# Performance work log

Hardware: AMD Instinct MI355X
Metric: run time of the kernel (lower is better)

The kernel has to match this reference:

```python
import jax, jax.numpy as jnp
import numpy as np
from jax import lax

B, H, W, Q, C = 2, 96, 96, 30000, 64
DIMS = [C * 9 + 4, 256, 256, 256, 256, 3]  # imnet MLP


def setup_inputs() -> dict:
    key = jax.random.key(0)
    ks = jax.random.split(key, 20)
    d = {}
    d["inp"] = jax.random.normal(ks[0], (B, 3, H, W), jnp.float32)
    d["coord"] = jax.random.uniform(ks[1], (B, Q, 2), jnp.float32) * 2.0 - 1.0
    d["cell"] = jax.random.uniform(ks[2], (B, Q, 2), jnp.float32) * (2.0 / 256.0)
    d["conv_w"] = jax.random.normal(ks[3], (C, 3, 3, 3), jnp.float32) * 0.1
    d["conv_b"] = jnp.zeros((C,), jnp.float32)
    for i in range(5):
        fan_in = DIMS[i]
        d[f"w{i}"] = jax.random.normal(ks[4 + i], (DIMS[i], DIMS[i + 1]), jnp.float32) / np.sqrt(fan_in)
        d[f"b{i}"] = jnp.zeros((DIMS[i + 1],), jnp.float32)
    return d


def _liif_forward(inp, coord, cell, conv_w, conv_b, ws, bs):
    # encoder: 3x3 conv + tanh (gen_feat)
    feat = lax.conv_general_dilated(inp, conv_w, (1, 1), "SAME",
                                    dimension_numbers=("NCHW", "OIHW", "NCHW"))
    feat = jnp.tanh(feat + conv_b[None, :, None, None])  # [B,C,H,W]
    b, c, h, w = feat.shape

    # feat_unfold: F.unfold(feat, 3, padding=1) -> [B, C*9, H, W]
    pad = jnp.pad(feat, ((0, 0), (0, 0), (1, 1), (1, 1)))
    patches = jnp.stack([pad[:, :, i:i + h, j:j + w] for i in range(3) for j in range(3)], axis=2)
    fu = patches.reshape(b, c * 9, h, w).transpose(0, 2, 3, 1)  # [B,H,W,9C]

    # local ensemble offsets
    offsets = jnp.array([[-1., -1.], [-1., 1.], [1., -1.], [1., 1.]], jnp.float32)
    rad = jnp.array([1.0 / h, 1.0 / w], jnp.float32)  # 2/r/2
    eps = 1e-6
    ec = coord[None] + (offsets * rad)[:, None, None, :] + eps  # [4,B,Q,2]
    ec = jnp.clip(ec, -1 + 1e-10, 1 - 1e-10)

    # grid_sample nearest, align_corners=False: ix = ((x+1)*size - 1)/2, round
    iy = jnp.clip(jnp.round((ec[..., 0] + 1) * h / 2 - 0.5).astype(jnp.int32), 0, h - 1)
    ix = jnp.clip(jnp.round((ec[..., 1] + 1) * w / 2 - 0.5).astype(jnp.int32), 0, w - 1)
    b_idx = jnp.arange(b)[None, :, None]  # [1,B,1]
    q_feat = fu[b_idx, iy, ix]  # [4,B,Q,9C]

    # feat_coord (make_coord): pixel-center coords in [-1,1]
    yc = (-1.0 + (2.0 * jnp.arange(h, dtype=jnp.float32) + 1.0) / h)
    xc = (-1.0 + (2.0 * jnp.arange(w, dtype=jnp.float32) + 1.0) / w)
    fc = jnp.stack(jnp.meshgrid(yc, xc, indexing="ij"), axis=-1)  # [H,W,2]
    q_coord = fc[iy, ix]  # [4,B,Q,2]

    scale = jnp.array([h, w], jnp.float32)
    rel_coord = (coord[None] - q_coord) * scale  # [4,B,Q,2]
    rel_cell = cell * scale  # [B,Q,2]

    x = jnp.concatenate(
        [q_feat, rel_coord, jnp.broadcast_to(rel_cell[None], rel_coord.shape)], axis=-1)  # [4,B,Q,580]

    # imnet MLP
    for wi, bi in zip(ws[:-1], bs[:-1]):
        x = jax.nn.relu(x @ wi + bi)
    x = x @ ws[-1] + bs[-1]  # [4,B,Q,3]

    areas = jnp.abs(jnp.prod(rel_coord, axis=-1, keepdims=True)) + 1e-9
    areas = areas / jnp.sum(areas, axis=0, keepdims=True)
    areas = areas[::-1]  # swap diagonal ensemble weights

    out = jnp.sum(x * areas, axis=0)  # [B,Q,3]
    return jnp.tanh(out) * 1.01  # fat_tanh(eps=0.01)


def reference(inp, coord, cell, conv_w, conv_b, w0, b0, w1, b1, w2, b2, w3, b3, w4, b4):
    return _liif_forward(inp, coord, cell, conv_w, conv_b,
                         [w0, w1, w2, w3, w4], [b0, b1, b2, b3, b4])
```

## Files before the change

kernel.cpp:

```cpp
#include <hip/hip_runtime.h>


typedef _Float16 half8   __attribute__((ext_vector_type(8)));
typedef _Float16 half4v  __attribute__((ext_vector_type(4)));
typedef _Float16 half2v  __attribute__((ext_vector_type(2)));
typedef float    float4v __attribute__((ext_vector_type(4)));
typedef float    floatx16 __attribute__((ext_vector_type(16)));

__device__ __forceinline__ _Float16 to_h(float v) {
  return (_Float16)fminf(fmaxf(v, -60000.0f), 60000.0f);
}

#define NQ 30000
#define QT 469
#define QTP 472

__global__ void prep_kernel(const float* __restrict__ w0,
                            const float* __restrict__ w1,
                            const float* __restrict__ w2,
                            const float* __restrict__ w3,
                            const float* __restrict__ w4,
                            _Float16* __restrict__ p0, _Float16* __restrict__ p1,
                            _Float16* __restrict__ p2, _Float16* __restrict__ p3,
                            _Float16* __restrict__ p4) {
  int idx = blockIdx.x * 256 + threadIdx.x;
  if (idx < 18944) {
    int kb = idx >> 8, n = idx & 255;
    half8 hv;
#pragma unroll
    for (int i = 0; i < 8; ++i) {
      int f = kb * 8 + i;
      float v = 0.0f;
      if (f < 576)      v = w0[((f & 63) * 9 + (f >> 6)) * 256 + n];
      else if (f < 580) v = w0[f * 256 + n];
      hv[i] = (_Float16)v;
    }
    *(half8*)(p0 + idx * 8) = hv;
  } else if (idx < 43520) {
    int j = idx - 18944;
    int l = j >> 13;
    int j2 = j & 8191;
    int kb = j2 >> 8, n = j2 & 255;
    const float* w = (l == 0) ? w1 : (l == 1) ? w2 : w3;
    _Float16* p = (l == 0) ? p1 : (l == 1) ? p2 : p3;
    half8 hv;
#pragma unroll
    for (int i = 0; i < 8; ++i)
      hv[i] = (_Float16)w[(kb * 8 + i) * 256 + n];
    *(half8*)(p + j2 * 8) = hv;
  } else if (idx < 44032) {
    int j = idx - 43520;
    int kb = j >> 4, n = j & 15;
    half8 hv;
#pragma unroll
    for (int i = 0; i < 8; ++i) {
      float v = (n < 3) ? w4[(kb * 8 + i) * 3 + n] : 0.0f;
      hv[i] = (_Float16)v;
    }
    *(half8*)(p4 + j * 8) = hv;
  }
}

__global__ void conv_kernel(const float* __restrict__ inp,
                            const float* __restrict__ cw,
                            const float* __restrict__ cb,
                            _Float16* __restrict__ P) {
  __shared__ __align__(16) float s_w[1728];
  __shared__ __align__(16) float s_b[64];
  for (int i = threadIdx.x; i < 1728; i += 256) s_w[i] = cw[i];
  if (threadIdx.x < 64) s_b[threadIdx.x] = cb[threadIdx.x];
  __syncthreads();
  int tid = blockIdx.x * 256 + threadIdx.x;
  if (tid >= 2 * 98 * 98) return;
  int b = tid / 9604;
  int rem = tid % 9604;
  int yy = rem / 98, xx = rem % 98;
  alignas(16) _Float16 outv[64];
  if (yy == 0 || yy == 97 || xx == 0 || xx == 97) {
#pragma unroll
    for (int c = 0; c < 64; ++c) outv[c] = (_Float16)0.0f;
  } else {
    int y = yy - 1, x = xx - 1;
    float win[27];
#pragma unroll
    for (int ci = 0; ci < 3; ++ci)
#pragma unroll
      for (int ky = 0; ky < 3; ++ky)
#pragma unroll
        for (int kx = 0; kx < 3; ++kx) {
          int yi = y + ky - 1, xi = x + kx - 1;
          float v = 0.0f;
          if (yi >= 0 && yi < 96 && xi >= 0 && xi < 96)
            v = inp[((b * 3 + ci) * 96 + yi) * 96 + xi];
          win[ci * 9 + ky * 3 + kx] = v;
        }
    for (int co = 0; co < 64; ++co) {
      float acc = s_b[co];
#pragma unroll
      for (int k = 0; k < 27; ++k) acc = fmaf(win[k], s_w[co * 27 + k], acc);
      outv[co] = (_Float16)tanhf(acc);
    }
  }
  _Float16* dst = P + tid * 64;
#pragma unroll
  for (int j = 0; j < 8; ++j) ((half8*)dst)[j] = ((const half8*)outv)[j];
}

__global__ __launch_bounds__(256, 1) void gmat_kernel(
    const _Float16* __restrict__ P,
    const _Float16* __restrict__ wp0,
    _Float16* __restrict__ G) {
  __shared__ __align__(16) _Float16 s_p[3][98][68];

  const int t    = threadIdx.x;
  const int lane = t & 63;
  const int wv   = t >> 6;
  const int ln32 = lane & 31;
  const int hi   = lane >> 5;
  const int blk  = blockIdx.x;
  const int bb   = (blk & 4) >> 2;
  const int y    = (blk >> 3) * 4 + (blk & 3);

  const int rowbase = (bb * 98 + y) * 98 * 64;
  for (int j = t; j < 2352; j += 256) {
    int row = j / 784;
    int jr  = j - row * 784;
    int px  = jr >> 3;
    int ci  = jr & 7;
    half8 v = *(const half8*)(P + rowbase + row * 6272 + jr * 8);
    *(half8*)(&s_p[row][px][ci * 8]) = v;
  }
  __syncthreads();

  const _Float16* wb0 = wp0 + (hi * 256 + wv * 64 + ln32) * 8;

  floatx16 acc[2][3];
#pragma unroll
  for (int mt2 = 0; mt2 < 2; ++mt2)
#pragma unroll
    for (int nt = 0; nt < 3; ++nt) acc[mt2][nt] = (floatx16)(0.0f);

  half8 afA[2], afB[2];
  afA[0] = *(const half8*)(wb0);          afA[1] = *(const half8*)(wb0 + 256);
  afB[0] = *(const half8*)(wb0 + 4096);   afB[1] = *(const half8*)(wb0 + 4096 + 256);

#pragma unroll 1
  for (int s = 0; s < 36; s += 2) {
    {
      const int patch = s >> 2;
      const int py = patch / 3, px = patch % 3;
      const int cb = ((s & 3) << 4) + hi * 8;
      half8 bf[3];
#pragma unroll
      for (int nt = 0; nt < 3; ++nt)
        bf[nt] = *(const half8*)(&s_p[py][nt * 32 + ln32 + px][cb]);
#pragma unroll
      for (int mt2 = 0; mt2 < 2; ++mt2)
#pragma unroll
        for (int nt = 0; nt < 3; ++nt)
          acc[mt2][nt] = __builtin_amdgcn_mfma_f32_32x32x16_f16(
              afA[mt2], bf[nt], acc[mt2][nt], 0, 0, 0);
      const int sp = (s + 2 <= 35) ? (s + 2) : 35;
      afA[0] = *(const half8*)(wb0 + sp * 4096);
      afA[1] = *(const half8*)(wb0 + sp * 4096 + 256);
    }
    {
      const int s1 = s + 1;
      const int patch = s1 >> 2;
      const int py = patch / 3, px = patch % 3;
      const int cb = ((s1 & 3) << 4) + hi * 8;
      half8 bf[3];
#pragma unroll
      for (int nt = 0; nt < 3; ++nt)
        bf[nt] = *(const half8*)(&s_p[py][nt * 32 + ln32 + px][cb]);
#pragma unroll
      for (int mt2 = 0; mt2 < 2; ++mt2)
#pragma unroll
        for (int nt = 0; nt < 3; ++nt)
          acc[mt2][nt] = __builtin_amdgcn_mfma_f32_32x32x16_f16(
              afB[mt2], bf[nt], acc[mt2][nt], 0, 0, 0);
      const int sp = (s + 3 <= 35) ? (s + 3) : 35;
      afB[0] = *(const half8*)(wb0 + sp * 4096);
      afB[1] = *(const half8*)(wb0 + sp * 4096 + 256);
    }
  }
  const int gybase = ((bb * 98 + y) * 98) * 256;
#pragma unroll
  for (int mt2 = 0; mt2 < 2; ++mt2)
#pragma unroll
    for (int nt = 0; nt < 3; ++nt) {
      half8 c0, c1;
#pragma unroll
      for (int j = 0; j < 8; ++j) {
        c0[j] = (_Float16)acc[mt2][nt][j];
        c1[j] = (_Float16)acc[mt2][nt][8 + j];
      }
      _Float16* ga = G + gybase + (nt * 32 + ln32) * 256 + (wv * 2 + mt2) * 32 + hi * 16;
      *(half8*)(ga)     = c0;
      *(half8*)(ga + 8) = c1;
    }
}

__device__ __forceinline__ void writeback32(floatx16 (&acc)[2][4],
                                            const float* __restrict__ sb,
                                            _Float16 (*s_h)[264],
                                            int wv, int ln32, int hi) {
#pragma unroll
  for (int mt2 = 0; mt2 < 2; ++mt2) {
    const int mb = wv * 64 + mt2 * 32 + 4 * hi;
#pragma unroll
    for (int g = 0; g < 4; ++g) {
      const int m0 = mb + 8 * g;
      float b0 = sb[m0], b1 = sb[m0 + 1], b2 = sb[m0 + 2], b3 = sb[m0 + 3];
#pragma unroll
      for (int nt2 = 0; nt2 < 4; ++nt2) {
        const int n = nt2 * 32 + ln32;
        float v0 = fmaxf(acc[mt2][nt2][4 * g + 0] + b0, 0.0f);
        float v1 = fmaxf(acc[mt2][nt2][4 * g + 1] + b1, 0.0f);
        float v2 = fmaxf(acc[mt2][nt2][4 * g + 2] + b2, 0.0f);
        float v3 = fmaxf(acc[mt2][nt2][4 * g + 3] + b3, 0.0f);
        half2v lo  = __builtin_bit_cast(half2v, __builtin_amdgcn_cvt_pkrtz(v0, v1));
        half2v hi2 = __builtin_bit_cast(half2v, __builtin_amdgcn_cvt_pkrtz(v2, v3));
        half4v hv;
        hv[0] = lo[0]; hv[1] = lo[1]; hv[2] = hi2[0]; hv[3] = hi2[1];
        *(half4v*)(&s_h[n][m0]) = hv;
      }
    }
  }
}

__device__ __forceinline__ void layer256(const _Float16* __restrict__ wbl,
                                         _Float16 (*s_h)[264],
                                         int ln32, int hi,
                                         floatx16 (&acc)[2][4]) {
#pragma unroll
  for (int mt2 = 0; mt2 < 2; ++mt2)
#pragma unroll
    for (int nt2 = 0; nt2 < 4; ++nt2) acc[mt2][nt2] = (floatx16)(0.0f);
  half8 afA[2], afB[2], bfA[4], bfB[4];
  afA[0] = *(const half8*)(wbl);
  afA[1] = *(const half8*)(wbl + 256);
  afB[0] = *(const half8*)(wbl + 4096);
  afB[1] = *(const half8*)(wbl + 4096 + 256);
#pragma unroll
  for (int nt2 = 0; nt2 < 4; ++nt2) {
    bfA[nt2] = *(const half8*)(&s_h[nt2 * 32 + ln32][hi * 8]);
    bfB[nt2] = *(const half8*)(&s_h[nt2 * 32 + ln32][16 + hi * 8]);
  }
#pragma unroll 1
  for (int s = 0; s < 16; s += 2) {
#pragma unroll
    for (int mt2 = 0; mt2 < 2; ++mt2)
#pragma unroll
      for (int nt2 = 0; nt2 < 4; ++nt2)
        acc[mt2][nt2] = __builtin_amdgcn_mfma_f32_32x32x16_f16(
            afA[mt2], bfA[nt2], acc[mt2][nt2], 0, 0, 0);
    {
      const int sc = (s + 2 < 16) ? (s + 2) : 0;
      const int sw = (s + 2 < 16) ? (s + 2) : 15;
      afA[0] = *(const half8*)(wbl + sw * 4096);
      afA[1] = *(const half8*)(wbl + sw * 4096 + 256);
#pragma unroll
      for (int nt2 = 0; nt2 < 4; ++nt2)
        bfA[nt2] = *(const half8*)(&s_h[nt2 * 32 + ln32][sc * 16 + hi * 8]);
    }
#pragma unroll
    for (int mt2 = 0; mt2 < 2; ++mt2)
#pragma unroll
      for (int nt2 = 0; nt2 < 4; ++nt2)
        acc[mt2][nt2] = __builtin_amdgcn_mfma_f32_32x32x16_f16(
            afB[mt2], bfB[nt2], acc[mt2][nt2], 0, 0, 0);
    {
      const int sc = (s + 3 < 16) ? (s + 3) : 0;
      const int sw = (s + 3 < 16) ? (s + 3) : 15;
      afB[0] = *(const half8*)(wbl + sw * 4096);
      afB[1] = *(const half8*)(wbl + sw * 4096 + 256);
#pragma unroll
      for (int nt2 = 0; nt2 < 4; ++nt2)
        bfB[nt2] = *(const half8*)(&s_h[nt2 * 32 + ln32][sc * 16 + hi * 8]);
    }
  }
}

__global__ __launch_bounds__(256, 2) void liif_main(
    const float* __restrict__ coord, const float* __restrict__ cell,
    const float* __restrict__ bias0, const float* __restrict__ bias1,
    const float* __restrict__ bias2, const float* __restrict__ bias3,
    const float* __restrict__ bias4,
    const _Float16* __restrict__ G,
    const _Float16* __restrict__ wp0, const _Float16* __restrict__ wp1,
    const _Float16* __restrict__ wp2, const _Float16* __restrict__ wp3,
    const _Float16* __restrict__ wp4,
    float* __restrict__ out) {
  __shared__ __align__(16) int      s_pix[4][64];
  __shared__ __align__(16) float    s_area[4][64];
  __shared__ __align__(16) _Float16 s_ext[4][64][8];
  __shared__ __align__(16) float    s_bias[1028];
  __shared__ __align__(16) float    s_out[128][4];
  __shared__ __align__(16) float    s_num[64][4];
  __shared__ __align__(16) _Float16 s_h[128][264];

  const int t   = threadIdx.x;
  const int blk = blockIdx.x;
  const int bb  = (blk & 4) >> 2;
  const int tile = (blk >> 3) * 4 + (blk & 3);
  const int q0  = tile * 64;

  for (int i = t; i < 1027; i += 256) {
    float v;
    if (i < 256)       v = bias0[i];
    else if (i < 512)  v = bias1[i - 256];
    else if (i < 768)  v = bias2[i - 512];
    else if (i < 1024) v = bias3[i - 768];
    else               v = bias4[i - 1024];
    s_bias[i] = v;
  }

  if (t < 64) {
    int q = q0 + t;
    bool valid = q < NQ;
    float c0 = 0.f, c1 = 0.f, e0 = 0.f, e1 = 0.f;
    if (valid) {
      int base = (bb * NQ + q) * 2;
      c0 = coord[base]; c1 = coord[base + 1];
      e0 = cell[base];  e1 = cell[base + 1];
    }
    float rc0 = e0 * 96.0f, rc1 = e1 * 96.0f;
#pragma unroll
    for (int o = 0; o < 4; ++o) {
      float oy = (o < 2) ? -1.0f : 1.0f;
      float ox = (o & 1) ? 1.0f : -1.0f;
      float ec0 = (c0 + oy * (1.0f / 96.0f)) + 1e-6f;
      float ec1 = (c1 + ox * (1.0f / 96.0f)) + 1e-6f;
      ec0 = fminf(fmaxf(ec0, -1.0f), 1.0f);
      ec1 = fminf(fmaxf(ec1, -1.0f), 1.0f);
      int iy = (int)rintf(((ec0 + 1.0f) * 96.0f) * 0.5f - 0.5f);
      int ix = (int)rintf(((ec1 + 1.0f) * 96.0f) * 0.5f - 0.5f);
      iy = min(max(iy, 0), 95); ix = min(max(ix, 0), 95);
      float qc0 = -1.0f + (2.0f * (float)iy + 1.0f) / 96.0f;
      float qc1 = -1.0f + (2.0f * (float)ix + 1.0f) / 96.0f;
      float r0 = (c0 - qc0) * 96.0f;
      float r1 = (c1 - qc1) * 96.0f;
      s_pix[o][t]  = (bb * 98 + iy) * 98 + ix;
      s_area[o][t] = fabsf(r0 * r1) + 1e-9f;
      s_ext[o][t][0] = to_h(r0);  s_ext[o][t][1] = to_h(r1);
      s_ext[o][t][2] = to_h(rc0); s_ext[o][t][3] = to_h(rc1);
      s_ext[o][t][4] = (_Float16)0.0f; s_ext[o][t][5] = (_Float16)0.0f;
      s_ext[o][t][6] = (_Float16)0.0f; s_ext[o][t][7] = (_Float16)0.0f;
    }
    s_num[t][0] = 0.f; s_num[t][1] = 0.f; s_num[t][2] = 0.f; s_num[t][3] = 0.f;
  }
  __syncthreads();

  const int lane = t & 63;
  const int wv   = t >> 6;
  const int ln32 = lane & 31;
  const int hi   = lane >> 5;
  const int ln16 = lane & 15;
  const int lg   = lane >> 4;

  const _Float16* wb0 = wp0 + (hi * 256 + wv * 64 + ln32) * 8;
  const _Float16* wb1 = wp1 + (hi * 256 + wv * 64 + ln32) * 8;
  const _Float16* wb2 = wp2 + (hi * 256 + wv * 64 + ln32) * 8;
  const _Float16* wb3 = wp3 + (hi * 256 + wv * 64 + ln32) * 8;

#pragma unroll 1
  for (int p = 0; p < 2; ++p) {
    int pixr[4]; int eidx[4];
#pragma unroll
    for (int nt2 = 0; nt2 < 4; ++nt2) {
      int r = nt2 * 32 + ln32;
      int o = p * 2 + (r >> 6);
      int q = r & 63;
      pixr[nt2] = s_pix[o][q];
      eidx[nt2] = (o * 64 + q) * 8;
    }

    floatx16 acc[2][4];
#pragma unroll
    for (int mt2 = 0; mt2 < 2; ++mt2)
#pragma unroll
      for (int nt2 = 0; nt2 < 4; ++nt2) {
        const _Float16* ga = G + pixr[nt2] * 256 + (wv * 2 + mt2) * 32 + hi * 16;
        half8 g0 = *(const half8*)(ga);
        half8 g1 = *(const half8*)(ga + 8);
        floatx16 a;
#pragma unroll
        for (int j = 0; j < 8; ++j) {
          a[j]     = (float)g0[j];
          a[8 + j] = (float)g1[j];
        }
        acc[mt2][nt2] = a;
      }
    {
      half8 ae[2];
      ae[0] = *(const half8*)(wb0 + 36 * 4096);
      ae[1] = *(const half8*)(wb0 + 36 * 4096 + 256);
      half8 z = {(_Float16)0, (_Float16)0, (_Float16)0, (_Float16)0,
                 (_Float16)0, (_Float16)0, (_Float16)0, (_Float16)0};
      half8 bfe[4];
#pragma unroll
      for (int nt2 = 0; nt2 < 4; ++nt2)
        bfe[nt2] = (hi == 0) ? *(const half8*)(&s_ext[0][0][0] + eidx[nt2]) : z;
#pragma unroll
      for (int mt2 = 0; mt2 < 2; ++mt2)
#pragma unroll
        for (int nt2 = 0; nt2 < 4; ++nt2)
          acc[mt2][nt2] = __builtin_amdgcn_mfma_f32_32x32x16_f16(
              ae[mt2], bfe[nt2], acc[mt2][nt2], 0, 0, 0);
    }
    writeback32(acc, s_bias, s_h, wv, ln32, hi);
    __syncthreads();

    layer256(wb1, s_h, ln32, hi, acc);
    __syncthreads();
    writeback32(acc, s_bias + 256, s_h, wv, ln32, hi);
    __syncthreads();

    layer256(wb2, s_h, ln32, hi, acc);
    __syncthreads();
    writeback32(acc, s_bias + 512, s_h, wv, ln32, hi);
    __syncthreads();

    layer256(wb3, s_h, ln32, hi, acc);
    __syncthreads();
    writeback32(acc, s_bias + 768, s_h, wv, ln32, hi);
    __syncthreads();

    half8 af4 = *(const half8*)(wp4 + (lg * 16 + ln16) * 8);
    float4v a4[2];
    a4[0] = (float4v){0.f, 0.f, 0.f, 0.f};
    a4[1] = (float4v){0.f, 0.f, 0.f, 0.f};
#pragma unroll 1
    for (int s = 0; s < 8; ++s) {
      half8 afc = af4;
      if (s < 7)
        af4 = *(const half8*)(wp4 + (((s + 1) * 4 + lg) * 16 + ln16) * 8);
#pragma unroll
      for (int u = 0; u < 2; ++u) {
        int row = (2 * wv + u) * 16 + ln16;
        half8 bf = *(const half8*)(&s_h[row][s * 32 + lg * 8]);
        a4[u] = __builtin_amdgcn_mfma_f32_16x16x32_f16(afc, bf, a4[u], 0, 0, 0);
      }
    }
    if (lg == 0) {
#pragma unroll
      for (int u = 0; u < 2; ++u) {
        int row = (2 * wv + u) * 16 + ln16;
        *(float4v*)(&s_out[row][0]) = a4[u];
      }
    }
    __syncthreads();

    if (t < 64) {
      float a_lo = s_area[3 - 2 * p][t];
      float a_hi = s_area[2 - 2 * p][t];
#pragma unroll
      for (int j = 0; j < 3; ++j)
        s_num[t][j] += s_out[t][j] * a_lo + s_out[64 + t][j] * a_hi;
    }
  }

  if (t < 64) {
    int q = q0 + t;
    if (q < NQ) {
      float den = s_area[0][t] + s_area[1][t] + s_area[2][t] + s_area[3][t];
      int ob = (bb * NQ + q) * 3;
#pragma unroll
      for (int j = 0; j < 3; ++j) {
        float v = s_num[t][j] / den + s_bias[1024 + j];
        out[ob + j] = tanhf(v) * 1.01f;
      }
    }
  }
}

extern "C" void kernel_launch(void* const* d_in, const int* in_sizes, int n_in,
                              void* d_out, int out_size, void* d_ws, size_t ws_size,
                              hipStream_t stream) {
  const float* inp   = (const float*)d_in[0];
  const float* coord = (const float*)d_in[1];
  const float* cell  = (const float*)d_in[2];
  const float* cw    = (const float*)d_in[3];
  const float* cb    = (const float*)d_in[4];
  const float* w0    = (const float*)d_in[5];
  const float* b0    = (const float*)d_in[6];
  const float* w1    = (const float*)d_in[7];
  const float* b1    = (const float*)d_in[8];
  const float* w2    = (const float*)d_in[9];
  const float* b2    = (const float*)d_in[10];
  const float* w3    = (const float*)d_in[11];
  const float* b3    = (const float*)d_in[12];
  const float* w4    = (const float*)d_in[13];
  const float* b4    = (const float*)d_in[14];

  char* ws = (char*)d_ws;
  _Float16* P   = (_Float16*)(ws);
  _Float16* wp0 = (_Float16*)(ws + 2458624);
  _Float16* wp1 = (_Float16*)(ws + 2761728);
  _Float16* wp2 = (_Float16*)(ws + 2892800);
  _Float16* wp3 = (_Float16*)(ws + 3023872);
  _Float16* wp4 = (_Float16*)(ws + 3154944);
  _Float16* G   = (_Float16*)(ws + 3163136);
  float* outp = (float*)d_out;

  hipLaunchKernelGGL(prep_kernel, dim3(172), dim3(256), 0, stream,
                     w0, w1, w2, w3, w4, wp0, wp1, wp2, wp3, wp4);
  hipLaunchKernelGGL(conv_kernel, dim3(76), dim3(256), 0, stream, inp, cw, cb, P);
  hipLaunchKernelGGL(gmat_kernel, dim3(192), dim3(256), 0, stream, P, wp0, G);
  hipLaunchKernelGGL(liif_main, dim3(8 * (QTP / 4)), dim3(256), 0, stream,
                     coord, cell, b0, b1, b2, b3, b4,
                     G, wp0, wp1, wp2, wp3, wp4, outp);
}
```

Before: 268.4 us.

## Process one ensemble offset per pass to halve tile and raise occupancy

Each MLP pass now covers 64 query rows (one ensemble offset) instead of 128 (two offsets), and the loop runs four times instead of two. Accumulator registers and the s_h/s_out shared buffers are halved, and launch bounds go from 2 to 3 blocks per SM. The aim is more resident waves to hide latency. The cost is double the barriers and loop iterations, and each weight fragment loaded is reused across fewer MFMAs.

```diff
diff --git a/kernel.cpp b/kernel.cpp
--- a/kernel.cpp
+++ b/kernel.cpp
@@ -201,7 +201,7 @@
     }
 }
 
-__device__ __forceinline__ void writeback32(floatx16 (&acc)[2][4],
+__device__ __forceinline__ void writeback32(floatx16 (&acc)[2][2],
                                             const float* __restrict__ sb,
                                             _Float16 (*s_h)[264],
                                             int wv, int ln32, int hi) {
@@ -213,7 +213,7 @@
       const int m0 = mb + 8 * g;
       float b0 = sb[m0], b1 = sb[m0 + 1], b2 = sb[m0 + 2], b3 = sb[m0 + 3];
 #pragma unroll
-      for (int nt2 = 0; nt2 < 4; ++nt2) {
+      for (int nt2 = 0; nt2 < 2; ++nt2) {
         const int n = nt2 * 32 + ln32;
         float v0 = fmaxf(acc[mt2][nt2][4 * g + 0] + b0, 0.0f);
         float v1 = fmaxf(acc[mt2][nt2][4 * g + 1] + b1, 0.0f);
@@ -232,18 +232,18 @@
 __device__ __forceinline__ void layer256(const _Float16* __restrict__ wbl,
                                          _Float16 (*s_h)[264],
                                          int ln32, int hi,
-                                         floatx16 (&acc)[2][4]) {
+                                         floatx16 (&acc)[2][2]) {
 #pragma unroll
   for (int mt2 = 0; mt2 < 2; ++mt2)
 #pragma unroll
-    for (int nt2 = 0; nt2 < 4; ++nt2) acc[mt2][nt2] = (floatx16)(0.0f);
-  half8 afA[2], afB[2], bfA[4], bfB[4];
+    for (int nt2 = 0; nt2 < 2; ++nt2) acc[mt2][nt2] = (floatx16)(0.0f);
+  half8 afA[2], afB[2], bfA[2], bfB[2];
   afA[0] = *(const half8*)(wbl);
   afA[1] = *(const half8*)(wbl + 256);
   afB[0] = *(const half8*)(wbl + 4096);
   afB[1] = *(const half8*)(wbl + 4096 + 256);
 #pragma unroll
-  for (int nt2 = 0; nt2 < 4; ++nt2) {
+  for (int nt2 = 0; nt2 < 2; ++nt2) {
     bfA[nt2] = *(const half8*)(&s_h[nt2 * 32 + ln32][hi * 8]);
     bfB[nt2] = *(const half8*)(&s_h[nt2 * 32 + ln32][16 + hi * 8]);
   }
@@ -252,7 +252,7 @@
 #pragma unroll
     for (int mt2 = 0; mt2 < 2; ++mt2)
 #pragma unroll
-      for (int nt2 = 0; nt2 < 4; ++nt2)
+      for (int nt2 = 0; nt2 < 2; ++nt2)
         acc[mt2][nt2] = __builtin_amdgcn_mfma_f32_32x32x16_f16(
             afA[mt2], bfA[nt2], acc[mt2][nt2], 0, 0, 0);
     {
@@ -261,13 +261,13 @@
       afA[0] = *(const half8*)(wbl + sw * 4096);
       afA[1] = *(const half8*)(wbl + sw * 4096 + 256);
 #pragma unroll
-      for (int nt2 = 0; nt2 < 4; ++nt2)
+      for (int nt2 = 0; nt2 < 2; ++nt2)
         bfA[nt2] = *(const half8*)(&s_h[nt2 * 32 + ln32][sc * 16 + hi * 8]);
     }
 #pragma unroll
     for (int mt2 = 0; mt2 < 2; ++mt2)
 #pragma unroll
-      for (int nt2 = 0; nt2 < 4; ++nt2)
+      for (int nt2 = 0; nt2 < 2; ++nt2)
         acc[mt2][nt2] = __builtin_amdgcn_mfma_f32_32x32x16_f16(
             afB[mt2], bfB[nt2], acc[mt2][nt2], 0, 0, 0);
     {
@@ -276,13 +276,13 @@
       afB[0] = *(const half8*)(wbl + sw * 4096);
       afB[1] = *(const half8*)(wbl + sw * 4096 + 256);
 #pragma unroll
-      for (int nt2 = 0; nt2 < 4; ++nt2)
+      for (int nt2 = 0; nt2 < 2; ++nt2)
         bfB[nt2] = *(const half8*)(&s_h[nt2 * 32 + ln32][sc * 16 + hi * 8]);
     }
   }
 }
 
-__global__ __launch_bounds__(256, 2) void liif_main(
+__global__ __launch_bounds__(256, 3) void liif_main(
     const float* __restrict__ coord, const float* __restrict__ cell,
     const float* __restrict__ bias0, const float* __restrict__ bias1,
     const float* __restrict__ bias2, const float* __restrict__ bias3,
@@ -296,9 +296,9 @@
   __shared__ __align__(16) float    s_area[4][64];
   __shared__ __align__(16) _Float16 s_ext[4][64][8];
   __shared__ __align__(16) float    s_bias[1028];
-  __shared__ __align__(16) float    s_out[128][4];
+  __shared__ __align__(16) float    s_out[64][4];
   __shared__ __align__(16) float    s_num[64][4];
-  __shared__ __align__(16) _Float16 s_h[128][264];
+  __shared__ __align__(16) _Float16 s_h[64][264];
 
   const int t   = threadIdx.x;
   const int blk = blockIdx.x;
@@ -365,22 +365,20 @@
   const _Float16* wb3 = wp3 + (hi * 256 + wv * 64 + ln32) * 8;
 
 #pragma unroll 1
-  for (int p = 0; p < 2; ++p) {
-    int pixr[4]; int eidx[4];
-#pragma unroll
-    for (int nt2 = 0; nt2 < 4; ++nt2) {
-      int r = nt2 * 32 + ln32;
-      int o = p * 2 + (r >> 6);
-      int q = r & 63;
-      pixr[nt2] = s_pix[o][q];
-      eidx[nt2] = (o * 64 + q) * 8;
-    }
-
-    floatx16 acc[2][4];
+  for (int p = 0; p < 4; ++p) {
+    int pixr[2]; int eidx[2];
+#pragma unroll
+    for (int nt2 = 0; nt2 < 2; ++nt2) {
+      int q = nt2 * 32 + ln32;
+      pixr[nt2] = s_pix[p][q];
+      eidx[nt2] = (p * 64 + q) * 8;
+    }
+
+    floatx16 acc[2][2];
 #pragma unroll
     for (int mt2 = 0; mt2 < 2; ++mt2)
 #pragma unroll
-      for (int nt2 = 0; nt2 < 4; ++nt2) {
+      for (int nt2 = 0; nt2 < 2; ++nt2) {
         const _Float16* ga = G + pixr[nt2] * 256 + (wv * 2 + mt2) * 32 + hi * 16;
         half8 g0 = *(const half8*)(ga);
         half8 g1 = *(const half8*)(ga + 8);
@@ -398,14 +396,14 @@
       ae[1] = *(const half8*)(wb0 + 36 * 4096 + 256);
       half8 z = {(_Float16)0, (_Float16)0, (_Float16)0, (_Float16)0,
                  (_Float16)0, (_Float16)0, (_Float16)0, (_Float16)0};
-      half8 bfe[4];
-#pragma unroll
-      for (int nt2 = 0; nt2 < 4; ++nt2)
+      half8 bfe[2];
+#pragma unroll
+      for (int nt2 = 0; nt2 < 2; ++nt2)
         bfe[nt2] = (hi == 0) ? *(const half8*)(&s_ext[0][0][0] + eidx[nt2]) : z;
 #pragma unroll
       for (int mt2 = 0; mt2 < 2; ++mt2)
 #pragma unroll
-        for (int nt2 = 0; nt2 < 4; ++nt2)
+        for (int nt2 = 0; nt2 < 2; ++nt2)
           acc[mt2][nt2] = __builtin_amdgcn_mfma_f32_32x32x16_f16(
               ae[mt2], bfe[nt2], acc[mt2][nt2], 0, 0, 0);
     }
@@ -428,36 +426,26 @@
     __syncthreads();
 
     half8 af4 = *(const half8*)(wp4 + (lg * 16 + ln16) * 8);
-    float4v a4[2];
-    a4[0] = (float4v){0.f, 0.f, 0.f, 0.f};
-    a4[1] = (float4v){0.f, 0.f, 0.f, 0.f};
+    float4v a4 = (float4v){0.f, 0.f, 0.f, 0.f};
+    const int row4 = wv * 16 + ln16;
 #pragma unroll 1
     for (int s = 0; s < 8; ++s) {
       half8 afc = af4;
       if (s < 7)
         af4 = *(const half8*)(wp4 + (((s + 1) * 4 + lg) * 16 + ln16) * 8);
-#pragma unroll
-      for (int u = 0; u < 2; ++u) {
-        int row = (2 * wv + u) * 16 + ln16;
-        half8 bf = *(const half8*)(&s_h[row][s * 32 + lg * 8]);
-        a4[u] = __builtin_amdgcn_mfma_f32_16x16x32_f16(afc, bf, a4[u], 0, 0, 0);
-      }
+      half8 bf = *(const half8*)(&s_h[row4][s * 32 + lg * 8]);
+      a4 = __builtin_amdgcn_mfma_f32_16x16x32_f16(afc, bf, a4, 0, 0, 0);
     }
     if (lg == 0) {
-#pragma unroll
-      for (int u = 0; u < 2; ++u) {
-        int row = (2 * wv + u) * 16 + ln16;
-        *(float4v*)(&s_out[row][0]) = a4[u];
-      }
+      *(float4v*)(&s_out[row4][0]) = a4;
     }
     __syncthreads();
 
     if (t < 64) {
-      float a_lo = s_area[3 - 2 * p][t];
-      float a_hi = s_area[2 - 2 * p][t];
+      float aw = s_area[3 - p][t];
 #pragma unroll
       for (int j = 0; j < 3; ++j)
-        s_num[t][j] += s_out[t][j] * a_lo + s_out[64 + t][j] * a_hi;
+        s_num[t][j] += s_out[t][j] * aw;
     }
   }
 
```

Result: slower. 301.6 us (+12.4%).
